# Kernel optimization log

Hardware: AMD Instinct MI355X
Metric: run time of the kernel (lower is better)

## Reference

```python
import jax, jax.numpy as jnp
import numpy as np

N_PROD, N_CUST = 100000, 50000
HID, OUT = 128, 64
E_PP, E_PC, E_LB = 800000, 800000, 400000


def sage(x_src, x_dst, src, dst, Wl, bl, Wr, n_dst):
    # PyG SAGEConv (mean aggr): lin_l(mean_{j->i} x_j) + lin_r(x_i); bias on lin_l only
    msg = x_src[src]                                             # [E, d] gather
    s = jax.ops.segment_sum(msg, dst, num_segments=n_dst)        # [n_dst, d]
    cnt = jax.ops.segment_sum(jnp.ones((src.shape[0],), x_src.dtype), dst, num_segments=n_dst)
    mean = s / jnp.maximum(cnt, 1.0)[:, None]
    return mean @ Wl.T + bl + x_dst @ Wr.T


def setup_inputs() -> dict:
    key = jax.random.key(0)
    ks = iter(jax.random.split(key, 40))

    def lin_w(i, o):
        return (jax.random.normal(next(ks), (o, i), jnp.float32) / np.sqrt(i))

    inp = {}
    inp['x_product'] = jax.random.normal(next(ks), (N_PROD, HID), jnp.float32)
    inp['x_customer'] = jax.random.normal(next(ks), (N_CUST, HID), jnp.float32)
    inp['ei_pp'] = jax.random.randint(next(ks), (2, E_PP), 0, N_PROD)
    src_pc = jax.random.randint(next(ks), (1, E_PC), 0, N_PROD)
    dst_pc = jax.random.randint(next(ks), (1, E_PC), 0, N_CUST)
    inp['ei_pc'] = jnp.concatenate([src_pc, dst_pc], axis=0)
    row = jax.random.randint(next(ks), (1, E_LB), 0, N_CUST)
    col = jax.random.randint(next(ks), (1, E_LB), 0, N_PROD)
    inp['edge_label_index'] = jnp.concatenate([row, col], axis=0)

    # ItemGNNEncoder params
    inp['it_W1l'], inp['it_W1r'] = lin_w(HID, HID), lin_w(HID, HID)
    inp['it_b1'] = jnp.zeros((HID,), jnp.float32)
    inp['it_W2l'], inp['it_W2r'] = lin_w(HID, HID), lin_w(HID, HID)
    inp['it_b2'] = jnp.zeros((HID,), jnp.float32)
    inp['it_Wlin'] = lin_w(HID, OUT)
    inp['it_blin'] = jnp.zeros((OUT,), jnp.float32)
    # UserGNNEncoder params
    inp['us_W1l'], inp['us_W1r'] = lin_w(HID, HID), lin_w(HID, HID)
    inp['us_b1'] = jnp.zeros((HID,), jnp.float32)
    inp['us_W2l'], inp['us_W2r'] = lin_w(HID, HID), lin_w(HID, HID)
    inp['us_b2'] = jnp.zeros((HID,), jnp.float32)
    inp['us_W3l'], inp['us_W3r'] = lin_w(HID, HID), lin_w(HID, HID)
    inp['us_b3'] = jnp.zeros((HID,), jnp.float32)
    inp['us_Wlin'] = lin_w(HID, OUT)
    inp['us_blin'] = jnp.zeros((OUT,), jnp.float32)
    # EdgeDecoder params
    inp['de_W1'] = lin_w(2 * OUT, OUT)
    inp['de_b1'] = jnp.zeros((OUT,), jnp.float32)
    inp['de_W2'] = lin_w(OUT, 1)
    inp['de_b2'] = jnp.zeros((1,), jnp.float32)
    return inp


def reference(x_product, x_customer, ei_pp, ei_pc, edge_label_index,
              it_W1l, it_b1, it_W1r, it_W2l, it_b2, it_W2r, it_Wlin, it_blin,
              us_W1l, us_b1, us_W1r, us_W2l, us_b2, us_W2r, us_W3l, us_b3, us_W3r,
              us_Wlin, us_blin, de_W1, de_b1, de_W2, de_b2):
    pp_s, pp_d = ei_pp[0], ei_pp[1]
    pc_s, pc_d = ei_pc[0], ei_pc[1]

    # ItemGNNEncoder on product-product metapath
    p = jax.nn.relu(sage(x_product, x_product, pp_s, pp_d, it_W1l, it_b1, it_W1r, N_PROD))
    p = jax.nn.relu(sage(p, p, pp_s, pp_d, it_W2l, it_b2, it_W2r, N_PROD))
    z_prod = p @ it_Wlin.T + it_blin                              # [N_PROD, OUT]

    # UserGNNEncoder
    px = jax.nn.relu(sage(x_product, x_product, pp_s, pp_d, us_W1l, us_b1, us_W1r, N_PROD))
    cx = jax.nn.relu(sage(x_product, x_customer, pc_s, pc_d, us_W2l, us_b2, us_W2r, N_CUST))
    cx = jax.nn.relu(sage(px, cx, pc_s, pc_d, us_W3l, us_b3, us_W3r, N_CUST))
    z_cust = cx @ us_Wlin.T + us_blin                             # [N_CUST, OUT]

    # EdgeDecoder: gather-concat-MLP
    row, col = edge_label_index[0], edge_label_index[1]
    z = jnp.concatenate([z_cust[row], z_prod[col]], axis=-1)      # [E_LB, 2*OUT]
    z = jax.nn.relu(z @ de_W1.T + de_b1)
    return z @ de_W2.T + de_b2                                    # [E_LB, 1]
```

## Files before the change

### kernel.cpp

```cpp
#include <hip/hip_runtime.h>
#include <hip/hip_bf16.h>

#define HID   128
#define OUTD  64
#define NPROD 100000
#define NCUST 50000
#define EPP   800000
#define EPC   800000
#define ELB   400000
#define NBK   391
#define EBLK  4096
#define RCAP3 512
#define BCAP3 2560
#define CPADN 400

typedef __bf16 bf16x8 __attribute__((ext_vector_type(8)));
typedef float  f32x4  __attribute__((ext_vector_type(4)));
typedef unsigned short u16;
typedef unsigned int u32;

__device__ __forceinline__ float b2f(u16 u) {
  unsigned int v = ((unsigned int)u) << 16;
  float f; __builtin_memcpy(&f, &v, 4); return f;
}
__device__ __forceinline__ u16 f2b(float f) {
  __hip_bfloat16 h = __float2bfloat16(f);
  u16 u; __builtin_memcpy(&u, &h, 2); return u;
}

union Pack8 { u16 u[8]; int4 v; };

__device__ __forceinline__ int sidx(int row, int chunk) {
  return row * HID + ((chunk ^ (row & 15)) << 3);
}
__device__ __forceinline__ int sidx64(int row, int chunk) {
  return row * 64 + ((chunk ^ (row & 7)) << 3);
}

__global__ __launch_bounds__(256) void k_cast(const float* __restrict__ src,
                                              u16* __restrict__ dst, int n8) {
  int i = blockIdx.x * 256 + threadIdx.x;
  if (i >= n8) return;
  float4 a = ((const float4*)src)[2 * i];
  float4 b = ((const float4*)src)[2 * i + 1];
  Pack8 p;
  p.u[0] = f2b(a.x); p.u[1] = f2b(a.y); p.u[2] = f2b(a.z); p.u[3] = f2b(a.w);
  p.u[4] = f2b(b.x); p.u[5] = f2b(b.y); p.u[6] = f2b(b.z); p.u[7] = f2b(b.w);
  ((int4*)dst)[i] = p.v;
}

#define NJOBS 13
struct CastJobs { const float* src[NJOBS]; int n8[NJOBS]; };

__global__ __launch_bounds__(256) void k_cast_w(CastJobs jobs, u16* __restrict__ wbuf) {
  int job = blockIdx.x >> 3;
  int idx = (blockIdx.x & 7) * 256 + threadIdx.x;
  int off8 = (job < 10) ? job * 2048 : 10 * 2048 + (job - 10) * 1024;
  if (idx >= jobs.n8[job]) return;
  const float* s = jobs.src[job];
  float4 a = ((const float4*)s)[2 * idx];
  float4 b = ((const float4*)s)[2 * idx + 1];
  Pack8 p;
  p.u[0] = f2b(a.x); p.u[1] = f2b(a.y); p.u[2] = f2b(a.z); p.u[3] = f2b(a.w);
  p.u[4] = f2b(b.x); p.u[5] = f2b(b.y); p.u[6] = f2b(b.z); p.u[7] = f2b(b.w);
  ((int4*)wbuf)[off8 + idx] = p.v;
}

__global__ __launch_bounds__(256) void k_bucket3(const int* __restrict__ ei_pp,
                                                 const int* __restrict__ ei_pc,
                                                 int* __restrict__ bfill_pp,
                                                 int* __restrict__ bfill_pc,
                                                 u32* __restrict__ bss_pp,
                                                 u32* __restrict__ bss_pc) {
  __shared__ int lcnt[NBK], lstart[NBK], lfill[NBK], gbase[NBK];
  __shared__ u32 spay[EBLK];
  __shared__ u16 sbk[EBLK];
  __shared__ int wtot[4];
  const int t = threadIdx.x;
  const int lane = t & 63, wv = t >> 6;
  int xcc; asm("s_getreg_b32 %0, hwreg(HW_REG_XCC_ID)" : "=s"(xcc));
  const int rep = xcc & 7;
  const int NBLK_PP = (EPP + EBLK - 1) / EBLK;
  const bool isPP = (int)blockIdx.x < NBLK_PP;
  const int* ei = isPP ? ei_pp : ei_pc;
  const int E  = isPP ? EPP : EPC;
  const int SH = isPP ? 8 : 7;
  int* bfill = isPP ? bfill_pp : bfill_pc;
  u32* bss   = isPP ? bss_pp : bss_pc;
  const int base = (isPP ? (int)blockIdx.x : (int)blockIdx.x - NBLK_PP) * EBLK;
  const int n = min(EBLK, E - base);

  for (int j = t; j < NBK; j += 256) { lcnt[j] = 0; lfill[j] = 0; }
  __syncthreads();

  u32 pay[16]; int bk[16];
  #pragma unroll
  for (int i = 0; i < 16; ++i) {
    int idx = i * 256 + t;
    bk[i] = -1;
    if (idx < n) {
      int e = base + idx;
      int s = ei[e];
      int d = ei[E + e];
      int b = d >> SH;
      bk[i] = b;
      pay[i] = ((u32)s << SH) | (u32)(d & ((1 << SH) - 1));
      atomicAdd(&lcnt[b], 1);
    }
  }
  __syncthreads();
  {
    int a0 = (2 * t < NBK) ? lcnt[2 * t] : 0;
    int a1 = (2 * t + 1 < NBK) ? lcnt[2 * t + 1] : 0;
    int s = a0 + a1;
    #pragma unroll
    for (int d = 1; d < 64; d <<= 1) {
      int u = __shfl_up(s, d, 64);
      if (lane >= d) s += u;
    }
    if (lane == 63) wtot[wv] = s;
    __syncthreads();
    int wpre = 0;
    for (int w = 0; w < wv; ++w) wpre += wtot[w];
    int excl = s + wpre - (a0 + a1);
    if (2 * t < NBK) lstart[2 * t] = excl;
    if (2 * t + 1 < NBK) lstart[2 * t + 1] = excl + a0;
  }
  __syncthreads();
  for (int b = t; b < NBK; b += 256) {
    int c = lcnt[b];
    gbase[b] = c ? atomicAdd(&bfill[(rep * CPADN + b) << 4], c) : 0;
  }
  #pragma unroll
  for (int i = 0; i < 16; ++i) {
    if (bk[i] >= 0) {
      int pos = lstart[bk[i]] + atomicAdd(&lfill[bk[i]], 1);
      spay[pos] = pay[i];
      sbk[pos] = (u16)bk[i];
    }
  }
  __syncthreads();
  for (int i = t; i < n; i += 256) {
    int b = sbk[i];
    int slot = gbase[b] + (i - lstart[b]);
    if (slot < RCAP3)
      bss[(b * 8 + rep) * RCAP3 + slot] = spay[i];
  }
}

template <int K, int SHL>
__global__ __launch_bounds__(256) void k_bsort(const u32* __restrict__ bss,
                                               const int* __restrict__ bfill,
                                               int* __restrict__ gctr,
                                               int* __restrict__ esrc,
                                               int* __restrict__ start,
                                               int* __restrict__ cnt,
                                               int n_nodes) {
  __shared__ u32 pairs[BCAP3];
  __shared__ int outsrc[BCAP3];
  __shared__ int lcnt[K], lstart[K], lfill[K];
  __shared__ int sh_n, sh_base, rn[8], roff[8];
  const int b = blockIdx.x, tid = threadIdx.x;
  if (tid < 8) rn[tid] = min(bfill[(tid * CPADN + b) << 4], RCAP3);
  for (int j = tid; j < K; j += 256) { lcnt[j] = 0; lfill[j] = 0; }
  __syncthreads();
  if (tid == 0) {
    int run = 0;
    for (int r = 0; r < 8; ++r) {
      roff[r] = run;
      int m = min(rn[r], BCAP3 - run);
      rn[r] = m;
      run += m;
    }
    sh_n = run;
    sh_base = atomicAdd(gctr, run);
  }
  __syncthreads();
  const int n = sh_n, base = sh_base;
  #pragma unroll
  for (int r = 0; r < 8; ++r) {
    int m = rn[r], o = roff[r];
    for (int i = tid; i < m; i += 256) {
      u32 p = bss[(b * 8 + r) * RCAP3 + i];
      pairs[o + i] = p;
      atomicAdd(&lcnt[p & (K - 1)], 1);
    }
  }
  __syncthreads();
  if (tid == 0) {
    int run = 0;
    for (int j = 0; j < K; ++j) { lstart[j] = run; run += lcnt[j]; }
  }
  __syncthreads();
  for (int i = tid; i < n; i += 256) {
    u32 p = pairs[i];
    int ln = p & (K - 1);
    int pos = lstart[ln] + atomicAdd(&lfill[ln], 1);
    outsrc[pos] = (int)(p >> SHL);
  }
  __syncthreads();
  for (int i = tid; i < n; i += 256) esrc[base + i] = outsrc[i];
  const int nb0 = b * K;
  for (int j = tid; j < K; j += 256) {
    int g = nb0 + j;
    if (g < n_nodes) { start[g] = base + lstart[j]; cnt[g] = lcnt[j]; }
  }
}

__global__ __launch_bounds__(256) void k_agg2(const int* __restrict__ es_a,
                                              const int* __restrict__ st_a,
                                              const int* __restrict__ cn_a,
                                              const u16* __restrict__ xa,
                                              u16* __restrict__ oa, int na,
                                              const int* __restrict__ es_b,
                                              const int* __restrict__ st_b,
                                              const int* __restrict__ cn_b,
                                              const u16* __restrict__ xb,
                                              u16* __restrict__ ob, int nb, int blkA) {
  const int t = threadIdx.x;
  const bool A = (int)blockIdx.x < blkA;
  const int node = (A ? (int)blockIdx.x : (int)blockIdx.x - blkA) * 16 + (t >> 4);
  const int l16 = t & 15;
  const int q4  = t & 48;
  if (node >= (A ? na : nb)) return;
  const int* esrc  = A ? es_a : es_b;
  const u16* x     = A ? xa : xb;
  u16* outm        = A ? oa : ob;
  int s0 = (A ? st_a : st_b)[node];
  int c  = (A ? cn_a : cn_b)[node];
  float acc[8] = {0.f, 0.f, 0.f, 0.f, 0.f, 0.f, 0.f, 0.f};
  for (int j0 = 0; j0 < c; j0 += 16) {
    int nch = min(16, c - j0);
    int eid = (l16 < nch) ? esrc[s0 + j0 + l16] : 0;
    int k = 0;
    for (; k + 4 <= nch; k += 4) {
      int s0i = __shfl(eid, q4 + k, 64);
      int s1i = __shfl(eid, q4 + k + 1, 64);
      int s2i = __shfl(eid, q4 + k + 2, 64);
      int s3i = __shfl(eid, q4 + k + 3, 64);
      Pack8 p0, p1, p2, p3;
      p0.v = *(const int4*)(x + (size_t)s0i * HID + l16 * 8);
      p1.v = *(const int4*)(x + (size_t)s1i * HID + l16 * 8);
      p2.v = *(const int4*)(x + (size_t)s2i * HID + l16 * 8);
      p3.v = *(const int4*)(x + (size_t)s3i * HID + l16 * 8);
      #pragma unroll
      for (int u = 0; u < 8; ++u)
        acc[u] += (b2f(p0.u[u]) + b2f(p1.u[u])) + (b2f(p2.u[u]) + b2f(p3.u[u]));
    }
    for (; k < nch; ++k) {
      int s = __shfl(eid, q4 + k, 64);
      Pack8 p;
      p.v = *(const int4*)(x + (size_t)s * HID + l16 * 8);
      #pragma unroll
      for (int u = 0; u < 8; ++u) acc[u] += b2f(p.u[u]);
    }
  }
  float inv = 1.0f / (float)max(c, 1);
  Pack8 o;
  #pragma unroll
  for (int u = 0; u < 8; ++u) o.u[u] = f2b(acc[u] * inv);
  *(int4*)(outm + (size_t)node * HID + l16 * 8) = o.v;
}

template <bool RELU, bool A2F, bool CHAIN, bool CHB>
__global__ __launch_bounds__(256) void k_gemm(const u16* __restrict__ A1,
                                              const u16* __restrict__ W1,
                                              const void* __restrict__ A2v,
                                              const u16* __restrict__ W2,
                                              const float* __restrict__ bias,
                                              u16* __restrict__ out, int M,
                                              const u16* __restrict__ Wlin,
                                              const float* __restrict__ blin,
                                              const u16* __restrict__ dW1,
                                              const float* __restrict__ db1) {
  __shared__ __align__(16) u16 sA[64 * HID];
  __shared__ __align__(16) u16 sW[128 * HID];
  const int tid  = threadIdx.x;
  const int lane = tid & 63;
  const int wave = tid >> 6;
  const int q    = lane >> 4;
  const int r16  = lane & 15;
  const int m0   = blockIdx.x * 64;

  f32x4 acc[4][2];
  #pragma unroll
  for (int i = 0; i < 4; ++i)
    #pragma unroll
    for (int j = 0; j < 2; ++j) {
      acc[i][j][0] = 0.f; acc[i][j][1] = 0.f; acc[i][j][2] = 0.f; acc[i][j][3] = 0.f;
    }

  #pragma unroll
  for (int phase = 0; phase < 2; ++phase) {
    const u16* W = phase ? W2 : W1;
    if (phase) __syncthreads();
    #pragma unroll
    for (int i = 0; i < 4; ++i) {
      int idx = i * 256 + tid;
      int rr = idx >> 4, c8 = idx & 15;
      int gr = m0 + rr;
      Pack8 p; p.v = make_int4(0, 0, 0, 0);
      if (gr < M) {
        if (phase == 0 || !A2F) {
          const u16* A = phase ? (const u16*)A2v : A1;
          p.v = *(const int4*)(A + (size_t)gr * HID + c8 * 8);
        } else {
          const float* A = (const float*)A2v;
          const float* s = A + (size_t)gr * HID + c8 * 8;
          float4 f0 = ((const float4*)s)[0], f1 = ((const float4*)s)[1];
          p.u[0] = f2b(f0.x); p.u[1] = f2b(f0.y); p.u[2] = f2b(f0.z); p.u[3] = f2b(f0.w);
          p.u[4] = f2b(f1.x); p.u[5] = f2b(f1.y); p.u[6] = f2b(f1.z); p.u[7] = f2b(f1.w);
        }
      }
      *(int4*)(sA + sidx(rr, c8)) = p.v;
    }
    #pragma unroll
    for (int i = 0; i < 8; ++i) {
      int idx = i * 256 + tid;
      int rr = idx >> 4, c8 = idx & 15;
      *(int4*)(sW + sidx(rr, c8)) = *(const int4*)(W + (size_t)rr * HID + c8 * 8);
    }
    __syncthreads();
    #pragma unroll
    for (int ks = 0; ks < 4; ++ks) {
      int chunk = ks * 4 + q;
      bf16x8 a[4], b[2];
      #pragma unroll
      for (int mi = 0; mi < 4; ++mi)
        a[mi] = *(const bf16x8*)(sA + sidx(mi * 16 + r16, chunk));
      #pragma unroll
      for (int ni = 0; ni < 2; ++ni)
        b[ni] = *(const bf16x8*)(sW + sidx(wave * 32 + ni * 16 + r16, chunk));
      #pragma unroll
      for (int mi = 0; mi < 4; ++mi)
        #pragma unroll
        for (int ni = 0; ni < 2; ++ni)
          acc[mi][ni] = __builtin_amdgcn_mfma_f32_16x16x32_bf16(a[mi], b[ni], acc[mi][ni], 0, 0, 0);
    }
  }

  if (!CHAIN) {
    #pragma unroll
    for (int ni = 0; ni < 2; ++ni) {
      int col = wave * 32 + ni * 16 + r16;
      float bv = bias[col];
      #pragma unroll
      for (int mi = 0; mi < 4; ++mi)
        #pragma unroll
        for (int r = 0; r < 4; ++r) {
          int gr = m0 + mi * 16 + q * 4 + r;
          if (gr < M) {
            float v = acc[mi][ni][r] + bv;
            if (RELU) v = fmaxf(v, 0.f);
            out[(size_t)gr * HID + col] = f2b(v);
          }
        }
    }
    return;
  }

  __syncthreads();
  #pragma unroll
  for (int ni = 0; ni < 2; ++ni) {
    int col = wave * 32 + ni * 16 + r16;
    float bv = bias[col];
    #pragma unroll
    for (int mi = 0; mi < 4; ++mi)
      #pragma unroll
      for (int r = 0; r < 4; ++r) {
        int rl = mi * 16 + q * 4 + r;
        float v = acc[mi][ni][r] + bv;
        if (RELU) v = fmaxf(v, 0.f);
        sA[rl * HID + (((col >> 3) ^ (rl & 15)) << 3) + (col & 7)] = f2b(v);
      }
  }
  #pragma unroll
  for (int i = 0; i < 4; ++i) {
    int idx = i * 256 + tid;
    int rr = idx >> 4, c8 = idx & 15;
    *(int4*)(sW + sidx(rr, c8)) = *(const int4*)(Wlin + (size_t)rr * HID + c8 * 8);
  }
  #pragma unroll
  for (int i = 0; i < 2; ++i) {
    int idx = i * 256 + tid;
    int rr = idx >> 3, c8 = idx & 7;
    *(int4*)(sW + 8192 + sidx64(rr, c8)) = *(const int4*)(dW1 + (size_t)rr * HID + c8 * 8);
  }
  __syncthreads();
  f32x4 az[4];
  #pragma unroll
  for (int i = 0; i < 4; ++i) { az[i][0]=0.f; az[i][1]=0.f; az[i][2]=0.f; az[i][3]=0.f; }
  #pragma unroll
  for (int ks = 0; ks < 4; ++ks) {
    int chunk = ks * 4 + q;
    bf16x8 b = *(const bf16x8*)(sW + sidx(wave * 16 + r16, chunk));
    #pragma unroll
    for (int mi = 0; mi < 4; ++mi) {
      bf16x8 a = *(const bf16x8*)(sA + sidx(mi * 16 + r16, chunk));
      az[mi] = __builtin_amdgcn_mfma_f32_16x16x32_bf16(a, b, az[mi], 0, 0, 0);
    }
  }
  {
    int col = wave * 16 + r16;
    float bl = blin[col];
    #pragma unroll
    for (int mi = 0; mi < 4; ++mi)
      #pragma unroll
      for (int r = 0; r < 4; ++r) {
        int rl = mi * 16 + q * 4 + r;
        sW[12288 + rl * 64 + (((col >> 3) ^ (rl & 7)) << 3) + (col & 7)] = f2b(az[mi][r] + bl);
      }
  }
  __syncthreads();
  f32x4 au[4];
  #pragma unroll
  for (int i = 0; i < 4; ++i) { au[i][0]=0.f; au[i][1]=0.f; au[i][2]=0.f; au[i][3]=0.f; }
  #pragma unroll
  for (int ks = 0; ks < 2; ++ks) {
    int chunk = ks * 4 + q;
    bf16x8 b = *(const bf16x8*)(sW + 8192 + sidx64(wave * 16 + r16, chunk));
    #pragma unroll
    for (int mi = 0; mi < 4; ++mi) {
      bf16x8 a = *(const bf16x8*)(sW + 12288 + sidx64(mi * 16 + r16, chunk));
      au[mi] = __builtin_amdgcn_mfma_f32_16x16x32_bf16(a, b, au[mi], 0, 0, 0);
    }
  }
  {
    int col = wave * 16 + r16;
    float db = CHB ? db1[col] : 0.f;
    #pragma unroll
    for (int mi = 0; mi < 4; ++mi)
      #pragma unroll
      for (int r = 0; r < 4; ++r) {
        int gr = m0 + mi * 16 + q * 4 + r;
        if (gr < M) out[(size_t)gr * 64 + col] = f2b(au[mi][r] + db);
      }
  }
}

__global__ __launch_bounds__(256) void k_edge(const u16* __restrict__ U,
                                              const u16* __restrict__ V,
                                              const int* __restrict__ eli,
                                              const float* __restrict__ w2,
                                              const float* __restrict__ b2,
                                              float* __restrict__ out) {
  const int lane = threadIdx.x & 63;
  const int wave = threadIdx.x >> 6;
  const int se   = (lane >> 3);
  const int ch   = lane & 7;
  float w2c[8];
  #pragma unroll
  for (int j = 0; j < 8; ++j) w2c[j] = w2[ch * 8 + j];
  const float b2v = b2[0];
  const int e0 = blockIdx.x * 256;
  #pragma unroll
  for (int p = 0; p < 8; ++p) {
    int e = e0 + p * 32 + wave * 8 + se;
    if (e < ELB) {
      int r = eli[e];
      int c = eli[ELB + e];
      Pack8 pu, pv;
      pu.v = *(const int4*)(U + (size_t)r * 64 + ch * 8);
      pv.v = *(const int4*)(V + (size_t)c * 64 + ch * 8);
      float s = 0.f;
      #pragma unroll
      for (int j = 0; j < 8; ++j)
        s += fmaxf(b2f(pu.u[j]) + b2f(pv.u[j]), 0.f) * w2c[j];
      s += __shfl_xor(s, 1, 64);
      s += __shfl_xor(s, 2, 64);
      s += __shfl_xor(s, 4, 64);
      if (ch == 0) out[e] = s + b2v;
    }
  }
}

extern "C" void kernel_launch(void* const* d_in, const int* in_sizes, int n_in,
                              void* d_out, int out_size, void* d_ws, size_t ws_size,
                              hipStream_t stream) {
  const float* x_prod = (const float*)d_in[0];
  const float* x_cust = (const float*)d_in[1];
  const int* ei_pp    = (const int*)d_in[2];
  const int* ei_pc    = (const int*)d_in[3];
  const int* eli      = (const int*)d_in[4];

  const float *it_W1l, *it_W1r, *it_b1, *it_W2l, *it_W2r, *it_b2, *it_Wlin, *it_blin;
  const float *us_W1l, *us_W1r, *us_b1, *us_W2l, *us_W2r, *us_b2;
  const float *us_W3l, *us_W3r, *us_b3, *us_Wlin, *us_blin;
  if (in_sizes[6] == 128) {
    it_W1l  = (const float*)d_in[5];  it_b1   = (const float*)d_in[6];  it_W1r  = (const float*)d_in[7];
    it_W2l  = (const float*)d_in[8];  it_b2   = (const float*)d_in[9];  it_W2r  = (const float*)d_in[10];
    it_Wlin = (const float*)d_in[11]; it_blin = (const float*)d_in[12];
    us_W1l  = (const float*)d_in[13]; us_b1   = (const float*)d_in[14]; us_W1r  = (const float*)d_in[15];
    us_W2l  = (const float*)d_in[16]; us_b2   = (const float*)d_in[17]; us_W2r  = (const float*)d_in[18];
    us_W3l  = (const float*)d_in[19]; us_b3   = (const float*)d_in[20]; us_W3r  = (const float*)d_in[21];
    us_Wlin = (const float*)d_in[22]; us_blin = (const float*)d_in[23];
  } else {
    it_W1l  = (const float*)d_in[5];  it_W1r  = (const float*)d_in[6];  it_b1   = (const float*)d_in[7];
    it_W2l  = (const float*)d_in[8];  it_W2r  = (const float*)d_in[9];  it_b2   = (const float*)d_in[10];
    it_Wlin = (const float*)d_in[11]; it_blin = (const float*)d_in[12];
    us_W1l  = (const float*)d_in[13]; us_W1r  = (const float*)d_in[14]; us_b1   = (const float*)d_in[15];
    us_W2l  = (const float*)d_in[16]; us_W2r  = (const float*)d_in[17]; us_b2   = (const float*)d_in[18];
    us_W3l  = (const float*)d_in[19]; us_W3r  = (const float*)d_in[20]; us_b3   = (const float*)d_in[21];
    us_Wlin = (const float*)d_in[22]; us_blin = (const float*)d_in[23];
  }
  const float* de_W1 = (const float*)d_in[24];
  const float* de_b1 = (const float*)d_in[25];
  const float* de_W2 = (const float*)d_in[26];
  const float* de_b2 = (const float*)d_in[27];

  char* ws = (char*)d_ws;
  int* bfill_pp = (int*)(ws + 0);
  int* bfill_pc = (int*)(ws + 409600);
  int* gctr     = (int*)(ws + 819200);
  int* start_pp = (int*)(ws + 819264);
  int* cnt_pp   = (int*)(ws + 1219264);
  int* start_pc = (int*)(ws + 1619264);
  int* cnt_pc   = (int*)(ws + 1819264);
  int* esrc_pp  = (int*)(ws + 2019264);
  int* esrc_pc  = (int*)(ws + 5219264);
  u16* wbuf  = (u16*)(ws + 8419264);
  u16* XPB   = (u16*)(ws + 8796096);
  u16* meanb = (u16*)(ws + 34396096);
  u16* P1    = (u16*)(ws + 59996096);
  u16* meanc = (u16*)(ws + 85596096);
  u16* CX    = (u16*)(ws + 98396096);
  u32* bss_pp = (u32*)P1;
  u32* bss_pc = (u32*)(ws + 59996096 + 6553600);
  u16* PX = XPB;
  u16* U  = (u16*)esrc_pp;
  u16* V  = CX;

  u16* w_it1l = wbuf + 0 * 16384;  u16* w_it1r = wbuf + 1 * 16384;
  u16* w_it2l = wbuf + 2 * 16384;  u16* w_it2r = wbuf + 3 * 16384;
  u16* w_us1l = wbuf + 4 * 16384;  u16* w_us1r = wbuf + 5 * 16384;
  u16* w_us2l = wbuf + 6 * 16384;  u16* w_us2r = wbuf + 7 * 16384;
  u16* w_us3l = wbuf + 8 * 16384;  u16* w_us3r = wbuf + 9 * 16384;
  u16* w_itlin = wbuf + 10 * 16384;
  u16* w_uslin = wbuf + 10 * 16384 + 8192;
  u16* w_deW1  = wbuf + 10 * 16384 + 2 * 8192;

  (void)n_in; (void)out_size; (void)ws_size;

  hipMemsetAsync(d_ws, 0, 819208, stream);

  dim3 B(256);
  k_cast<<<dim3((NPROD * HID / 8 + 255) / 256), B, 0, stream>>>(x_prod, XPB, NPROD * HID / 8);
  CastJobs jobs;
  jobs.src[0] = it_W1l;  jobs.src[1] = it_W1r;  jobs.src[2] = it_W2l;  jobs.src[3] = it_W2r;
  jobs.src[4] = us_W1l;  jobs.src[5] = us_W1r;  jobs.src[6] = us_W2l;  jobs.src[7] = us_W2r;
  jobs.src[8] = us_W3l;  jobs.src[9] = us_W3r;
  jobs.src[10] = it_Wlin; jobs.src[11] = us_Wlin; jobs.src[12] = de_W1;
  for (int i = 0; i < 10; ++i) jobs.n8[i] = 2048;
  for (int i = 10; i < 13; ++i) jobs.n8[i] = 1024;
  k_cast_w<<<dim3(NJOBS * 8), B, 0, stream>>>(jobs, wbuf);

  const int NBLK_PP = (EPP + EBLK - 1) / EBLK;
  const int NBLK_PC = (EPC + EBLK - 1) / EBLK;
  k_bucket3<<<dim3(NBLK_PP + NBLK_PC), B, 0, stream>>>(ei_pp, ei_pc, bfill_pp, bfill_pc,
                                                       bss_pp, bss_pc);
  k_bsort<256, 8><<<dim3(NBK), B, 0, stream>>>(bss_pp, bfill_pp, gctr, esrc_pp, start_pp, cnt_pp, NPROD);
  k_bsort<128, 7><<<dim3(NBK), B, 0, stream>>>(bss_pc, bfill_pc, gctr + 1, esrc_pc, start_pc, cnt_pc, NCUST);

  dim3 Gp((NPROD + 63) / 64), Gc((NCUST + 63) / 64);
  const int App = (NPROD + 15) / 16, Apc = (NCUST + 15) / 16;

  k_agg2<<<dim3(App + Apc), B, 0, stream>>>(esrc_pp, start_pp, cnt_pp, XPB, meanb, NPROD,
                                            esrc_pc, start_pc, cnt_pc, XPB, meanc, NCUST, App);
  k_gemm<true, true, false, false><<<Gc, B, 0, stream>>>(
      meanc, w_us2l, x_cust, w_us2r, us_b2, CX, NCUST, nullptr, nullptr, nullptr, nullptr);
  k_gemm<true, false, false, false><<<Gp, B, 0, stream>>>(
      meanb, w_it1l, XPB, w_it1r, it_b1, P1, NPROD, nullptr, nullptr, nullptr, nullptr);
  k_gemm<true, false, false, false><<<Gp, B, 0, stream>>>(
      meanb, w_us1l, XPB, w_us1r, us_b1, PX, NPROD, nullptr, nullptr, nullptr, nullptr);
  k_agg2<<<dim3(App + Apc), B, 0, stream>>>(esrc_pp, start_pp, cnt_pp, P1, meanb, NPROD,
                                            esrc_pc, start_pc, cnt_pc, PX, meanc, NCUST, App);
  k_gemm<true, false, true, true><<<Gc, B, 0, stream>>>(
      meanc, w_us3l, CX, w_us3r, us_b3, U, NCUST, w_uslin, us_blin, w_deW1, de_b1);
  k_gemm<true, false, true, false><<<Gp, B, 0, stream>>>(
      meanb, w_it2l, P1, w_it2r, it_b2, V, NPROD, w_itlin, it_blin, w_deW1 + 64, nullptr);
  k_edge<<<dim3((ELB + 255) / 256), B, 0, stream>>>(U, V, eli, de_W2, de_b2, (float*)d_out);
}
```

Before: 523.7 us.

## Split neighbor aggregation by feature chunk so each block touches a narrow column slice

The mean-aggregation kernel is restructured so each block handles one 16-column chunk of 128 nodes, with two threads per node each loading 8 bf16 values. All blocks on a chunk gather from the same narrow column slice of the source features, which is meant to improve cache locality. Edge indices are now read per thread with nontemporal loads instead of being shared through wave shuffles, and outputs are written with nontemporal stores. The second aggregation is split into two launches instead of one combined launch. The cost is redundant index reads (8x across chunks) and more launches.

```diff
diff --git a/kernel.cpp b/kernel.cpp
--- a/kernel.cpp
+++ b/kernel.cpp
@@ -16,6 +16,7 @@
 
 typedef __bf16 bf16x8 __attribute__((ext_vector_type(8)));
 typedef float  f32x4  __attribute__((ext_vector_type(4)));
+typedef int    i32x4  __attribute__((ext_vector_type(4)));
 typedef unsigned short u16;
 typedef unsigned int u32;
 
@@ -28,7 +29,7 @@
   u16 u; __builtin_memcpy(&u, &h, 2); return u;
 }
 
-union Pack8 { u16 u[8]; int4 v; };
+union Pack8 { u16 u[8]; int4 v; i32x4 cv; };
 
 __device__ __forceinline__ int sidx(int row, int chunk) {
   return row * HID + ((chunk ^ (row & 15)) << 3);
@@ -207,59 +208,59 @@
   }
 }
 
-__global__ __launch_bounds__(256) void k_agg2(const int* __restrict__ es_a,
+__global__ __launch_bounds__(256) void k_agg3(const int* __restrict__ es_a,
                                               const int* __restrict__ st_a,
                                               const int* __restrict__ cn_a,
                                               const u16* __restrict__ xa,
-                                              u16* __restrict__ oa, int na,
+                                              u16* __restrict__ oa, int ga, int na,
                                               const int* __restrict__ es_b,
                                               const int* __restrict__ st_b,
                                               const int* __restrict__ cn_b,
                                               const u16* __restrict__ xb,
-                                              u16* __restrict__ ob, int nb, int blkA) {
+                                              u16* __restrict__ ob, int nb) {
   const int t = threadIdx.x;
-  const bool A = (int)blockIdx.x < blkA;
-  const int node = (A ? (int)blockIdx.x : (int)blockIdx.x - blkA) * 16 + (t >> 4);
-  const int l16 = t & 15;
-  const int q4  = t & 48;
+  const int chunk = blockIdx.x & 7;
+  const int grp = blockIdx.x >> 3;
+  const bool A = grp < ga;
+  const int g = A ? grp : grp - ga;
+  const int node = g * 128 + (t >> 1);
+  const int half = t & 1;
   if (node >= (A ? na : nb)) return;
-  const int* esrc  = A ? es_a : es_b;
-  const u16* x     = A ? xa : xb;
-  u16* outm        = A ? oa : ob;
-  int s0 = (A ? st_a : st_b)[node];
-  int c  = (A ? cn_a : cn_b)[node];
+  const int* es = A ? es_a : es_b;
+  const u16* x  = A ? xa : xb;
+  u16* o        = A ? oa : ob;
+  const int s0 = __builtin_nontemporal_load((A ? st_a : st_b) + node);
+  const int c  = __builtin_nontemporal_load((A ? cn_a : cn_b) + node);
+  const u16* xc = x + chunk * 16 + half * 8;
+
   float acc[8] = {0.f, 0.f, 0.f, 0.f, 0.f, 0.f, 0.f, 0.f};
-  for (int j0 = 0; j0 < c; j0 += 16) {
-    int nch = min(16, c - j0);
-    int eid = (l16 < nch) ? esrc[s0 + j0 + l16] : 0;
-    int k = 0;
-    for (; k + 4 <= nch; k += 4) {
-      int s0i = __shfl(eid, q4 + k, 64);
-      int s1i = __shfl(eid, q4 + k + 1, 64);
-      int s2i = __shfl(eid, q4 + k + 2, 64);
-      int s3i = __shfl(eid, q4 + k + 3, 64);
-      Pack8 p0, p1, p2, p3;
-      p0.v = *(const int4*)(x + (size_t)s0i * HID + l16 * 8);
-      p1.v = *(const int4*)(x + (size_t)s1i * HID + l16 * 8);
-      p2.v = *(const int4*)(x + (size_t)s2i * HID + l16 * 8);
-      p3.v = *(const int4*)(x + (size_t)s3i * HID + l16 * 8);
-      #pragma unroll
-      for (int u = 0; u < 8; ++u)
-        acc[u] += (b2f(p0.u[u]) + b2f(p1.u[u])) + (b2f(p2.u[u]) + b2f(p3.u[u]));
-    }
-    for (; k < nch; ++k) {
-      int s = __shfl(eid, q4 + k, 64);
-      Pack8 p;
-      p.v = *(const int4*)(x + (size_t)s * HID + l16 * 8);
-      #pragma unroll
-      for (int u = 0; u < 8; ++u) acc[u] += b2f(p.u[u]);
-    }
+  int j = 0;
+  for (; j + 4 <= c; j += 4) {
+    int i0 = __builtin_nontemporal_load(es + s0 + j);
+    int i1 = __builtin_nontemporal_load(es + s0 + j + 1);
+    int i2 = __builtin_nontemporal_load(es + s0 + j + 2);
+    int i3 = __builtin_nontemporal_load(es + s0 + j + 3);
+    Pack8 p0, p1, p2, p3;
+    p0.v = *(const int4*)(xc + (size_t)i0 * HID);
+    p1.v = *(const int4*)(xc + (size_t)i1 * HID);
+    p2.v = *(const int4*)(xc + (size_t)i2 * HID);
+    p3.v = *(const int4*)(xc + (size_t)i3 * HID);
+    #pragma unroll
+    for (int u = 0; u < 8; ++u)
+      acc[u] += (b2f(p0.u[u]) + b2f(p1.u[u])) + (b2f(p2.u[u]) + b2f(p3.u[u]));
+  }
+  for (; j < c; ++j) {
+    int i0 = __builtin_nontemporal_load(es + s0 + j);
+    Pack8 p;
+    p.v = *(const int4*)(xc + (size_t)i0 * HID);
+    #pragma unroll
+    for (int u = 0; u < 8; ++u) acc[u] += b2f(p.u[u]);
   }
   float inv = 1.0f / (float)max(c, 1);
-  Pack8 o;
-  #pragma unroll
-  for (int u = 0; u < 8; ++u) o.u[u] = f2b(acc[u] * inv);
-  *(int4*)(outm + (size_t)node * HID + l16 * 8) = o.v;
+  Pack8 po;
+  #pragma unroll
+  for (int u = 0; u < 8; ++u) po.u[u] = f2b(acc[u] * inv);
+  __builtin_nontemporal_store(po.cv, (i32x4*)(o + (size_t)node * HID + chunk * 16 + half * 8));
 }
 
 template <bool RELU, bool A2F, bool CHAIN, bool CHB>
@@ -562,18 +563,24 @@
   k_bsort<128, 7><<<dim3(NBK), B, 0, stream>>>(bss_pc, bfill_pc, gctr + 1, esrc_pc, start_pc, cnt_pc, NCUST);
 
   dim3 Gp((NPROD + 63) / 64), Gc((NCUST + 63) / 64);
-  const int App = (NPROD + 15) / 16, Apc = (NCUST + 15) / 16;
-
-  k_agg2<<<dim3(App + Apc), B, 0, stream>>>(esrc_pp, start_pp, cnt_pp, XPB, meanb, NPROD,
-                                            esrc_pc, start_pc, cnt_pc, XPB, meanc, NCUST, App);
+  const int GAp = (NPROD + 127) / 128;
+  const int GAc = (NCUST + 127) / 128;
+
+  k_agg3<<<dim3((GAp + GAc) * 8), B, 0, stream>>>(
+      esrc_pp, start_pp, cnt_pp, XPB, meanb, GAp, NPROD,
+      esrc_pc, start_pc, cnt_pc, XPB, meanc, NCUST);
   k_gemm<true, true, false, false><<<Gc, B, 0, stream>>>(
       meanc, w_us2l, x_cust, w_us2r, us_b2, CX, NCUST, nullptr, nullptr, nullptr, nullptr);
   k_gemm<true, false, false, false><<<Gp, B, 0, stream>>>(
       meanb, w_it1l, XPB, w_it1r, it_b1, P1, NPROD, nullptr, nullptr, nullptr, nullptr);
   k_gemm<true, false, false, false><<<Gp, B, 0, stream>>>(
       meanb, w_us1l, XPB, w_us1r, us_b1, PX, NPROD, nullptr, nullptr, nullptr, nullptr);
-  k_agg2<<<dim3(App + Apc), B, 0, stream>>>(esrc_pp, start_pp, cnt_pp, P1, meanb, NPROD,
-                                            esrc_pc, start_pc, cnt_pc, PX, meanc, NCUST, App);
+  k_agg3<<<dim3(GAp * 8), B, 0, stream>>>(
+      esrc_pp, start_pp, cnt_pp, P1, meanb, GAp, NPROD,
+      esrc_pc, start_pc, cnt_pc, PX, meanc, NCUST);
+  k_agg3<<<dim3(GAc * 8), B, 0, stream>>>(
+      esrc_pc, start_pc, cnt_pc, PX, meanc, GAc, NCUST,
+      esrc_pp, start_pp, cnt_pp, P1, meanb, NPROD);
   k_gemm<true, false, true, true><<<Gc, B, 0, stream>>>(
       meanc, w_us3l, CX, w_us3r, us_b3, U, NCUST, w_uslin, us_blin, w_deW1, de_b1);
   k_gemm<true, false, true, false><<<Gp, B, 0, stream>>>(
```

Result: slower. 807.7 us (+54.2%).
